# Kernel tuning notes

Hardware: AMD Instinct MI355X
Metric: run time of the kernel (lower is better)

## Reference

```python
import jax, jax.numpy as jnp
import numpy as np

B, L, D, H = 2, 2048, 1024, 16
DH = D // H
TAU = 0.1


def setup_inputs() -> dict:
    key = jax.random.key(0)
    ks = jax.random.split(key, 12)
    s = 0.02
    return {
        "q_x": jax.random.normal(ks[0], (B, L, D), jnp.float32),
        "k_x": jax.random.normal(ks[1], (B, L, D), jnp.float32),
        "v_x": jax.random.normal(ks[2], (B, L, D), jnp.float32),
        "ec": jax.random.normal(ks[3], (B, L, D), jnp.float32),
        "Wq": jax.random.normal(ks[4], (D, D), jnp.float32) * s,
        "bq": jnp.zeros((D,), jnp.float32),
        "Wk": jax.random.normal(ks[5], (D, D), jnp.float32) * s,
        "bk": jnp.zeros((D,), jnp.float32),
        "Wv": jax.random.normal(ks[6], (D, D), jnp.float32) * s,
        "bv": jnp.zeros((D,), jnp.float32),
        "Wo": jax.random.normal(ks[7], (D, D), jnp.float32) * s,
        "bo": jnp.zeros((D,), jnp.float32),
    }


def reference(q_x, k_x, v_x, ec, Wq, bq, Wk, bk, Wv, bv, Wo, bo):
    # torch nn.Linear: y = x @ W.T + b
    Q = (q_x @ Wq.T + bq).reshape(B, L, H, DH).transpose(0, 2, 1, 3)   # [B,H,L,Dh]
    K = (k_x @ Wk.T + bk).reshape(B, -1, H, DH).transpose(0, 2, 1, 3)  # [B,H,S,Dh]
    V = (v_x @ Wv.T + bv).reshape(B, -1, H, DH).transpose(0, 2, 1, 3)  # [B,H,S,Dh]
    scores = jnp.einsum("bhld,bhsd->bhls", Q, K) / jnp.sqrt(jnp.float32(DH))
    w = jnp.nan_to_num(jax.nn.softmax(scores, axis=-1), nan=0.0)       # [B,H,L,S]
    # frequency gate per key position: sigmoid((mean|ec| - tau) * 10)
    gate = jax.nn.sigmoid((jnp.abs(ec).mean(-1) - TAU) * 10.0)          # [B,S]
    w = w * gate[:, None, None, :]
    out = jnp.einsum("bhls,bhsd->bhld", w, V)                           # [B,H,L,Dh]
    out = out.transpose(0, 2, 1, 3).reshape(B, L, D)
    return out @ Wo.T + bo
```

## Files before the change

kernel.cpp:

```cpp
#include <hip/hip_runtime.h>

typedef unsigned short u16;
typedef unsigned int u32;
typedef unsigned long long u64;
typedef __attribute__((ext_vector_type(8))) short bf16x8;
typedef __attribute__((ext_vector_type(4))) float f32x4;
typedef __attribute__((ext_vector_type(2))) unsigned int u32x2;
typedef __attribute__((ext_vector_type(4))) unsigned int u32x4;

#define B_ 2
#define L_ 2048
#define D_ 1024
#define H_ 16
#define M_ 4096

__device__ __forceinline__ u16 f2bf(float f) {
  u32 x = __builtin_bit_cast(u32, f);
  return (u16)((x + 0x7fffu + ((x >> 16) & 1u)) >> 16);
}
__device__ __forceinline__ u32 cvtpk(float lo, float hi) {
  u32 r;
  asm("v_cvt_pk_bf16_f32 %0, %1, %2" : "=v"(r) : "v"(lo), "v"(hi));
  return r;
}

__device__ __forceinline__ void lane_regroup(u32& a, u32& b) {
#if __has_builtin(__builtin_amdgcn_permlane32_swap) && \
    __has_builtin(__builtin_amdgcn_permlane16_swap)
  u32x2 r = __builtin_amdgcn_permlane32_swap(a, b, false, false);
  u32x2 t = __builtin_amdgcn_permlane16_swap(r.x, r.y, false, false);
  a = t.x;
  b = t.y;
#else
  asm("v_permlane32_swap_b32 %0, %1\n\t"
      "v_permlane16_swap_b32 %0, %1"
      : "+v"(a), "+v"(b));
#endif
}

__device__ __forceinline__ void gl2lds16(void* lds, const void* g) {
  __builtin_amdgcn_global_load_lds(
      (const __attribute__((address_space(1))) u32*)g,
      (__attribute__((address_space(3))) u32*)lds, 16, 0, 0);
}

__device__ __forceinline__ void wait_vm8() {
  asm volatile("s_waitcnt vmcnt(8)" ::: "memory");
}
__device__ __forceinline__ void wait_vm0() {
  asm volatile("s_waitcnt vmcnt(0)" ::: "memory");
}
__device__ __forceinline__ void bar() {
  asm volatile("" ::: "memory");
  __builtin_amdgcn_s_barrier();
  asm volatile("" ::: "memory");
}

__global__ void cvt_all(const float* __restrict__ q, const float* __restrict__ k,
                        const float* __restrict__ v, const float* __restrict__ wq,
                        const float* __restrict__ wk, const float* __restrict__ wv,
                        const float* __restrict__ wo, const float* __restrict__ ec,
                        u16* __restrict__ Xq, u16* __restrict__ Xk, u16* __restrict__ Xv,
                        u16* __restrict__ Wqb, u16* __restrict__ Wkb,
                        u16* __restrict__ Wvb, u16* __restrict__ Wob,
                        float* __restrict__ gate) {
  if (blockIdx.x >= 16384) {
    int row = (blockIdx.x - 16384) * 4 + (threadIdx.x >> 6);
    int lane = threadIdx.x & 63;
    const float4* p = (const float4*)(ec + (size_t)row * 1024);
    float s = 0.f;
#pragma unroll
    for (int i = 0; i < 4; i++) {
      float4 vv = p[i * 64 + lane];
      s += fabsf(vv.x) + fabsf(vv.y) + fabsf(vv.z) + fabsf(vv.w);
    }
#pragma unroll
    for (int m = 1; m < 64; m <<= 1) s += __shfl_xor(s, m);
    if (lane == 0) {
      float mean = s * (1.0f / 1024.0f);
      gate[row] = 1.0f / (1.0f + __expf(-(mean - 0.1f) * 10.0f));
    }
    return;
  }
  int i = blockIdx.x * 256 + threadIdx.x;
  const float* s;
  u16* d;
  int off;
  if (i < 3145728) {
    int t = i >> 20;
    off = i & 1048575;
    s = t == 0 ? q : t == 1 ? k : v;
    d = t == 0 ? Xq : t == 1 ? Xk : Xv;
  } else {
    int j = i - 3145728;
    int t = j >> 18;
    off = j & 262143;
    s = t == 0 ? wq : t == 1 ? wk : t == 2 ? wv : wo;
    d = t == 0 ? Wqb : t == 1 ? Wkb : t == 2 ? Wvb : Wob;
  }
  float4 vv = ((const float4*)s)[off];
  ((u64*)d)[off] = (u64)cvtpk(vv.x, vv.y) | ((u64)cvtpk(vv.z, vv.w) << 32);
}

__global__ __launch_bounds__(256, 2) void gemm_qkv(
    const u16* __restrict__ Xq, const u16* __restrict__ Xk, const u16* __restrict__ Xv,
    const u16* __restrict__ Wq, const u16* __restrict__ Wk, const u16* __restrict__ Wv,
    const float* __restrict__ bq, const float* __restrict__ bk,
    const float* __restrict__ bv, const float* __restrict__ gate,
    u16* __restrict__ Qo, u16* __restrict__ Ko, u16* __restrict__ Vt) {
  __shared__ char smem[65536];
  const int which = blockIdx.x >> 8;
  const u16* A = which == 0 ? Xq : which == 1 ? Xk : Xv;
  const u16* Bw = which == 0 ? Wq : which == 1 ? Wk : Wv;
  const float* bias = which == 0 ? bq : which == 1 ? bk : bv;
  const int bi = blockIdx.x & 255;
  const int tid = threadIdx.x;
  const int tm = bi >> 3;
  const int tn = bi & 7;
  const int w = tid >> 6, lane = tid & 63;
  const int c = lane & 15, g = lane >> 4;
  const int wr = (w >> 1) << 6, wc = (w & 1) << 6;
  const int srow = tid >> 3, sch = tid & 7;

  f32x4 acc[4][4] = {};

  auto stage = [&](int buf, int t) {
    char* As = smem + buf * 32768;
    char* Bs = As + 16384;
#pragma unroll
    for (int i = 0; i < 4; i++) {
      int row = i * 32 + srow;
      int chs = (sch ^ (row & 7)) << 3;
      gl2lds16(As + i * 4096 + w * 1024, A + (size_t)(tm * 128 + row) * 1024 + t * 64 + chs);
      gl2lds16(Bs + i * 4096 + w * 1024, Bw + (size_t)(tn * 128 + row) * 1024 + t * 64 + chs);
    }
  };

  stage(0, 0);
  for (int t = 0; t < 16; t++) {
    int cur = t & 1;
    if (t < 15) {
      stage(cur ^ 1, t + 1);
      wait_vm8();
    } else {
      wait_vm0();
    }
    bar();
    const char* As = smem + cur * 32768;
    const char* Bs = As + 16384;
#pragma unroll
    for (int kd = 0; kd < 2; kd++) {
      bf16x8 af[4], bfr[4];
#pragma unroll
      for (int fi = 0; fi < 4; fi++) {
        int ra = wr + fi * 16 + c;
        af[fi] = *(const bf16x8*)(As + ra * 128 + ((((kd << 2) | g) ^ (ra & 7)) << 4));
        int rb = wc + fi * 16 + c;
        bfr[fi] = *(const bf16x8*)(Bs + rb * 128 + ((((kd << 2) | g) ^ (rb & 7)) << 4));
      }
#pragma unroll
      for (int fi = 0; fi < 4; fi++)
#pragma unroll
        for (int fj = 0; fj < 4; fj++)
          acc[fi][fj] = __builtin_amdgcn_mfma_f32_16x16x32_bf16(af[fi], bfr[fj],
                                                                acc[fi][fj], 0, 0, 0);
    }
    bar();
  }

  if (which == 2) {
    u16* T = (u16*)smem;
    __syncthreads();
#pragma unroll
    for (int fi = 0; fi < 4; fi++) {
      int lr0 = wr + fi * 16 + g * 4;
      float4 gg = *(const float4*)(gate + tm * 128 + lr0);
#pragma unroll
      for (int fj = 0; fj < 4; fj++) {
        int lc = wc + fj * 16 + c;
        float bv2 = bias[tn * 128 + lc];
        T[lc * 136 + lr0 + 0] = f2bf((acc[fi][fj][0] + bv2) * gg.x);
        T[lc * 136 + lr0 + 1] = f2bf((acc[fi][fj][1] + bv2) * gg.y);
        T[lc * 136 + lr0 + 2] = f2bf((acc[fi][fj][2] + bv2) * gg.z);
        T[lc * 136 + lr0 + 3] = f2bf((acc[fi][fj][3] + bv2) * gg.w);
      }
    }
    __syncthreads();
    const int lc = tid >> 1, hf = tid & 1;
    const int vtrow = (tm >> 4) * 1024 + tn * 128 + lc;
    const int s0 = (tm & 15) * 128 + hf * 64;
    const char* Trow = (const char*)(T + lc * 136) + hf * 128;
    u16* dst = Vt + (size_t)vtrow * 2048 + s0;
#pragma unroll
    for (int j = 0; j < 8; j++)
      *(bf16x8*)(dst + j * 8) = *(const bf16x8*)(Trow + j * 16);
  } else {
    u16* Cout = which == 0 ? Qo : Ko;
    const float oscl = which == 0 ? 0.18033688011112042f : 1.0f;
    const int rowb = tm * 128 + wr + g * 4;
    const int colb = tn * 128 + wc + c;
#pragma unroll
    for (int fj = 0; fj < 4; fj++) {
      int col = colb + fj * 16;
      float bv2 = bias[col];
#pragma unroll
      for (int fi = 0; fi < 4; fi++) {
        int r0 = rowb + fi * 16;
#pragma unroll
        for (int r = 0; r < 4; r++)
          Cout[(size_t)(r0 + r) * 1024 + col] = f2bf((acc[fi][fj][r] + bv2) * oscl);
      }
    }
  }
}

__global__ __launch_bounds__(256, 2) void gemm_o(const u16* __restrict__ A,
                                                 const u16* __restrict__ Bw,
                                                 const float* __restrict__ bias,
                                                 float* __restrict__ Cout) {
  __shared__ char smem[65536];
  const int tid = threadIdx.x;
  const int tm = blockIdx.x >> 3;
  const int tn = blockIdx.x & 7;
  const int w = tid >> 6, lane = tid & 63;
  const int c = lane & 15, g = lane >> 4;
  const int wr = (w >> 1) << 6, wc = (w & 1) << 6;
  const int srow = tid >> 3, sch = tid & 7;

  f32x4 acc[4][4] = {};

  auto stage = [&](int buf, int t) {
    char* As = smem + buf * 32768;
    char* Bs = As + 16384;
#pragma unroll
    for (int i = 0; i < 4; i++) {
      int row = i * 32 + srow;
      int chs = (sch ^ (row & 7)) << 3;
      gl2lds16(As + i * 4096 + w * 1024, A + (size_t)(tm * 128 + row) * 1024 + t * 64 + chs);
      gl2lds16(Bs + i * 4096 + w * 1024, Bw + (size_t)(tn * 128 + row) * 1024 + t * 64 + chs);
    }
  };

  stage(0, 0);
  for (int t = 0; t < 16; t++) {
    int cur = t & 1;
    if (t < 15) {
      stage(cur ^ 1, t + 1);
      wait_vm8();
    } else {
      wait_vm0();
    }
    bar();
    const char* As = smem + cur * 32768;
    const char* Bs = As + 16384;
#pragma unroll
    for (int kd = 0; kd < 2; kd++) {
      bf16x8 af[4], bfr[4];
#pragma unroll
      for (int fi = 0; fi < 4; fi++) {
        int ra = wr + fi * 16 + c;
        af[fi] = *(const bf16x8*)(As + ra * 128 + ((((kd << 2) | g) ^ (ra & 7)) << 4));
        int rb = wc + fi * 16 + c;
        bfr[fi] = *(const bf16x8*)(Bs + rb * 128 + ((((kd << 2) | g) ^ (rb & 7)) << 4));
      }
#pragma unroll
      for (int fi = 0; fi < 4; fi++)
#pragma unroll
        for (int fj = 0; fj < 4; fj++)
          acc[fi][fj] = __builtin_amdgcn_mfma_f32_16x16x32_bf16(af[fi], bfr[fj],
                                                                acc[fi][fj], 0, 0, 0);
    }
    bar();
  }

  const int rowb = tm * 128 + wr + g * 4;
  const int colb = tn * 128 + wc + c;
#pragma unroll
  for (int fj = 0; fj < 4; fj++) {
    int col = colb + fj * 16;
    float bv2 = bias[col];
#pragma unroll
    for (int fi = 0; fi < 4; fi++) {
      int r0 = rowb + fi * 16;
#pragma unroll
      for (int r = 0; r < 4; r++)
        Cout[(size_t)(r0 + r) * 1024 + col] = acc[fi][fj][r] + bv2;
    }
  }
}

__global__ __launch_bounds__(256, 2) void attn_kernel(const u16* __restrict__ Qb,
                                                      const u16* __restrict__ Kb,
                                                      const u16* __restrict__ Vt,
                                                      u16* __restrict__ Ob) {
  __shared__ char asmem[65536];
  const int bi = blockIdx.x;
  const int bh = (bi & 7) | ((bi >> 7) << 3);
  const int qt = (bi >> 3) & 15;
  const int b = bh >> 4, h = bh & 15;
  const int tid = threadIdx.x, w = tid >> 6, lane = tid & 63;
  const int c = lane & 15, g = lane >> 4;
  const int qrow0 = b * L_ + qt * 128 + w * 32;

  bf16x8 qf[2][2];
#pragma unroll
  for (int fj = 0; fj < 2; fj++)
#pragma unroll
    for (int kd = 0; kd < 2; kd++)
      qf[fj][kd] = *(const bf16x8*)(Qb + (size_t)(qrow0 + fj * 16 + c) * D_ + h * 64 +
                                    kd * 32 + g * 8);

  float lsum[2] = {0.f, 0.f};
  f32x4 oacc[4][2] = {};

  const int srow = tid >> 3, sch = tid & 7;
  const int vrow = tid >> 4, vch = tid & 15;

  auto stage = [&](int buf, int kv) {
    char* KsB = asmem + buf * 32768;
    char* VsB = KsB + 16384;
    int sbase = kv * 128;
#pragma unroll
    for (int i = 0; i < 4; i++) {
      int kr = i * 32 + srow;
      gl2lds16(KsB + i * 4096 + w * 1024,
               Kb + (size_t)(b * L_ + sbase + kr) * D_ + h * 64 + ((sch ^ (kr & 7)) << 3));
      int vr = i * 16 + vrow;
      gl2lds16(VsB + i * 4096 + w * 1024,
               Vt + (size_t)(bh * 64 + vr) * 2048 + sbase + ((vch ^ (vr & 15)) << 3));
    }
  };

  stage(0, 0);
  for (int kv = 0; kv < 16; kv++) {
    int cur = kv & 1;
    if (kv < 15) {
      stage(cur ^ 1, kv + 1);
      wait_vm8();
    } else {
      wait_vm0();
    }
    bar();
    const char* Ks = asmem + cur * 32768;
    const char* Vs = Ks + 16384;

    f32x4 st0[8] = {}, st1[8] = {};
    __builtin_amdgcn_s_setprio(1);
#pragma unroll
    for (int kd = 0; kd < 2; kd++) {
#pragma unroll
      for (int fi = 0; fi < 8; fi++) {
        int row = fi * 16 + c;
        bf16x8 kf = *(const bf16x8*)(Ks + row * 128 + ((((kd << 2) | g) ^ (c & 7)) << 4));
        st0[fi] = __builtin_amdgcn_mfma_f32_16x16x32_bf16(kf, qf[0][kd], st0[fi], 0, 0, 0);
        st1[fi] = __builtin_amdgcn_mfma_f32_16x16x32_bf16(kf, qf[1][kd], st1[fi], 0, 0, 0);
      }
    }
    __builtin_amdgcn_s_setprio(0);

    u32 pkA0[8], pkB0[8], pkA1[8], pkB1[8];
    float rs0 = 0.f, rs1 = 0.f;
#pragma unroll
    for (int fi = 0; fi < 8; fi++) {
      float p0 = __builtin_amdgcn_exp2f(st0[fi][0]);
      float p1 = __builtin_amdgcn_exp2f(st0[fi][1]);
      float p2 = __builtin_amdgcn_exp2f(st0[fi][2]);
      float p3 = __builtin_amdgcn_exp2f(st0[fi][3]);
      rs0 += (p0 + p1) + (p2 + p3);
      pkA0[fi] = cvtpk(p0, p1);
      pkB0[fi] = cvtpk(p2, p3);
    }
#pragma unroll
    for (int fi = 0; fi < 8; fi++) {
      float p0 = __builtin_amdgcn_exp2f(st1[fi][0]);
      float p1 = __builtin_amdgcn_exp2f(st1[fi][1]);
      float p2 = __builtin_amdgcn_exp2f(st1[fi][2]);
      float p3 = __builtin_amdgcn_exp2f(st1[fi][3]);
      rs1 += (p0 + p1) + (p2 + p3);
      pkA1[fi] = cvtpk(p0, p1);
      pkB1[fi] = cvtpk(p2, p3);
    }
    lsum[0] += rs0;
    lsum[1] += rs1;

    __builtin_amdgcn_s_setprio(1);
#pragma unroll
    for (int ks = 0; ks < 4; ks++) {
      u32 a0 = pkA0[2 * ks], b0 = pkA0[2 * ks + 1];
      lane_regroup(a0, b0);
      u32 a1 = pkB0[2 * ks], b1 = pkB0[2 * ks + 1];
      lane_regroup(a1, b1);
      u32x4 pw0 = {a0, a1, b0, b1};
      bf16x8 pf0 = __builtin_bit_cast(bf16x8, pw0);
      u32 e0 = pkA1[2 * ks], f0 = pkA1[2 * ks + 1];
      lane_regroup(e0, f0);
      u32 e1 = pkB1[2 * ks], f1 = pkB1[2 * ks + 1];
      lane_regroup(e1, f1);
      u32x4 pw1 = {e0, e1, f0, f1};
      bf16x8 pf1 = __builtin_bit_cast(bf16x8, pw1);
#pragma unroll
      for (int fd = 0; fd < 4; fd++) {
        int vr2 = fd * 16 + c;
        bf16x8 vf = *(const bf16x8*)(Vs + vr2 * 256 + ((((ks << 2) | g) ^ (vr2 & 15)) << 4));
        oacc[fd][0] = __builtin_amdgcn_mfma_f32_16x16x32_bf16(vf, pf0, oacc[fd][0], 0, 0, 0);
        oacc[fd][1] = __builtin_amdgcn_mfma_f32_16x16x32_bf16(vf, pf1, oacc[fd][1], 0, 0, 0);
      }
    }
    __builtin_amdgcn_s_setprio(0);
    bar();
  }

#pragma unroll
  for (int fj = 0; fj < 2; fj++) {
    lsum[fj] += __shfl_xor(lsum[fj], 16);
    lsum[fj] += __shfl_xor(lsum[fj], 32);
    float inv = 1.0f / lsum[fj];
    size_t orow = (size_t)(qrow0 + fj * 16 + c) * D_ + h * 64;
#pragma unroll
    for (int fd = 0; fd < 4; fd++) {
      u64 pk = (u64)cvtpk(oacc[fd][fj][0] * inv, oacc[fd][fj][1] * inv) |
               ((u64)cvtpk(oacc[fd][fj][2] * inv, oacc[fd][fj][3] * inv) << 32);
      *(u64*)(Ob + orow + fd * 16 + g * 4) = pk;
    }
  }
}

extern "C" void kernel_launch(void* const* d_in, const int* in_sizes, int n_in,
                              void* d_out, int out_size, void* d_ws, size_t ws_size,
                              hipStream_t stream) {
  const float* q_x = (const float*)d_in[0];
  const float* k_x = (const float*)d_in[1];
  const float* v_x = (const float*)d_in[2];
  const float* ec = (const float*)d_in[3];
  const float* Wq = (const float*)d_in[4];
  const float* bq = (const float*)d_in[5];
  const float* Wk = (const float*)d_in[6];
  const float* bk = (const float*)d_in[7];
  const float* Wv = (const float*)d_in[8];
  const float* bv = (const float*)d_in[9];
  const float* Wo = (const float*)d_in[10];
  const float* bo = (const float*)d_in[11];

  char* ws = (char*)d_ws;
  const size_t MB = 1024 * 1024;
  u16* Wqb = (u16*)(ws + 0 * MB);
  u16* Wkb = (u16*)(ws + 2 * MB);
  u16* Wvb = (u16*)(ws + 4 * MB);
  u16* Wob = (u16*)(ws + 6 * MB);
  float* gatep = (float*)(ws + 8 * MB);
  u16* Xq = (u16*)(ws + 9 * MB);
  u16* Xk = (u16*)(ws + 17 * MB);
  u16* Xv = (u16*)(ws + 25 * MB);
  u16* Qb = (u16*)(ws + 33 * MB);
  u16* Kb = (u16*)(ws + 41 * MB);
  u16* Vtb = (u16*)(ws + 49 * MB);
  u16* Ab = Xk;

  cvt_all<<<17408, 256, 0, stream>>>(q_x, k_x, v_x, Wq, Wk, Wv, Wo, ec, Xq, Xk, Xv,
                                     Wqb, Wkb, Wvb, Wob, gatep);
  gemm_qkv<<<768, 256, 0, stream>>>(Xq, Xk, Xv, Wqb, Wkb, Wvb, bq, bk, bv, gatep, Qb,
                                    Kb, Vtb);
  attn_kernel<<<512, 256, 0, stream>>>(Qb, Kb, Vtb, Ab);
  gemm_o<<<256, 256, 0, stream>>>(Ab, Wob, bo, (float*)d_out);
}
```

Measured before the change: 115.5 us.

## Halve gemm_o M-tile and compute softmax row sums with ones-MFMA

The output projection GEMM now uses 64x128 tiles with 512 blocks instead of 128x128 tiles with 256 blocks, so more CUs are busy on the 4096x1024 output. Its LDS use and per-wave accumulators shrink, and the vmcnt wait threshold is adjusted to match. In attention, the per-lane exp row-sum accumulation and the cross-lane shuffles are replaced by an extra MFMA per step that multiplies the bf16 probabilities by a vector of ones. This takes VALU adds off the softmax path but sums the bf16-rounded probabilities, which changes numerics slightly, and it reduces reuse of the GEMM tile.

```diff
diff --git a/kernel.cpp b/kernel.cpp
--- a/kernel.cpp
+++ b/kernel.cpp
@@ -46,6 +46,9 @@
 
 __device__ __forceinline__ void wait_vm8() {
   asm volatile("s_waitcnt vmcnt(8)" ::: "memory");
+}
+__device__ __forceinline__ void wait_vm6() {
+  asm volatile("s_waitcnt vmcnt(6)" ::: "memory");
 }
 __device__ __forceinline__ void wait_vm0() {
   asm volatile("s_waitcnt vmcnt(0)" ::: "memory");
@@ -218,25 +221,31 @@
                                                  const u16* __restrict__ Bw,
                                                  const float* __restrict__ bias,
                                                  float* __restrict__ Cout) {
-  __shared__ char smem[65536];
+  __shared__ char smem[49152];
   const int tid = threadIdx.x;
   const int tm = blockIdx.x >> 3;
   const int tn = blockIdx.x & 7;
   const int w = tid >> 6, lane = tid & 63;
   const int c = lane & 15, g = lane >> 4;
-  const int wr = (w >> 1) << 6, wc = (w & 1) << 6;
+  const int wr = (w >> 1) << 5;
+  const int wc = (w & 1) << 6;
   const int srow = tid >> 3, sch = tid & 7;
 
-  f32x4 acc[4][4] = {};
+  f32x4 acc[2][4] = {};
 
   auto stage = [&](int buf, int t) {
-    char* As = smem + buf * 32768;
-    char* Bs = As + 16384;
+    char* As = smem + buf * 24576;
+    char* Bs = As + 8192;
+#pragma unroll
+    for (int i = 0; i < 2; i++) {
+      int row = i * 32 + srow;
+      int chs = (sch ^ (row & 7)) << 3;
+      gl2lds16(As + i * 4096 + w * 1024, A + (size_t)(tm * 64 + row) * 1024 + t * 64 + chs);
+    }
 #pragma unroll
     for (int i = 0; i < 4; i++) {
       int row = i * 32 + srow;
       int chs = (sch ^ (row & 7)) << 3;
-      gl2lds16(As + i * 4096 + w * 1024, A + (size_t)(tm * 128 + row) * 1024 + t * 64 + chs);
       gl2lds16(Bs + i * 4096 + w * 1024, Bw + (size_t)(tn * 128 + row) * 1024 + t * 64 + chs);
     }
   };
@@ -246,25 +255,28 @@
     int cur = t & 1;
     if (t < 15) {
       stage(cur ^ 1, t + 1);
-      wait_vm8();
+      wait_vm6();
     } else {
       wait_vm0();
     }
     bar();
-    const char* As = smem + cur * 32768;
-    const char* Bs = As + 16384;
+    const char* As = smem + cur * 24576;
+    const char* Bs = As + 8192;
 #pragma unroll
     for (int kd = 0; kd < 2; kd++) {
-      bf16x8 af[4], bfr[4];
-#pragma unroll
-      for (int fi = 0; fi < 4; fi++) {
+      bf16x8 af[2], bfr[4];
+#pragma unroll
+      for (int fi = 0; fi < 2; fi++) {
         int ra = wr + fi * 16 + c;
         af[fi] = *(const bf16x8*)(As + ra * 128 + ((((kd << 2) | g) ^ (ra & 7)) << 4));
-        int rb = wc + fi * 16 + c;
-        bfr[fi] = *(const bf16x8*)(Bs + rb * 128 + ((((kd << 2) | g) ^ (rb & 7)) << 4));
-      }
-#pragma unroll
-      for (int fi = 0; fi < 4; fi++)
+      }
+#pragma unroll
+      for (int fj = 0; fj < 4; fj++) {
+        int rb = wc + fj * 16 + c;
+        bfr[fj] = *(const bf16x8*)(Bs + rb * 128 + ((((kd << 2) | g) ^ (rb & 7)) << 4));
+      }
+#pragma unroll
+      for (int fi = 0; fi < 2; fi++)
 #pragma unroll
         for (int fj = 0; fj < 4; fj++)
           acc[fi][fj] = __builtin_amdgcn_mfma_f32_16x16x32_bf16(af[fi], bfr[fj],
@@ -273,14 +285,14 @@
     bar();
   }
 
-  const int rowb = tm * 128 + wr + g * 4;
+  const int rowb = tm * 64 + wr + g * 4;
   const int colb = tn * 128 + wc + c;
 #pragma unroll
   for (int fj = 0; fj < 4; fj++) {
     int col = colb + fj * 16;
     float bv2 = bias[col];
 #pragma unroll
-    for (int fi = 0; fi < 4; fi++) {
+    for (int fi = 0; fi < 2; fi++) {
       int r0 = rowb + fi * 16;
 #pragma unroll
       for (int r = 0; r < 4; r++)
@@ -310,8 +322,11 @@
       qf[fj][kd] = *(const bf16x8*)(Qb + (size_t)(qrow0 + fj * 16 + c) * D_ + h * 64 +
                                     kd * 32 + g * 8);
 
-  float lsum[2] = {0.f, 0.f};
+  const u32x4 onew = {0x3F803F80u, 0x3F803F80u, 0x3F803F80u, 0x3F803F80u};
+  const bf16x8 one8 = __builtin_bit_cast(bf16x8, onew);
+
   f32x4 oacc[4][2] = {};
+  f32x4 oaccD[2] = {};
 
   const int srow = tid >> 3, sch = tid & 7;
   const int vrow = tid >> 4, vch = tid & 15;
@@ -359,29 +374,16 @@
     __builtin_amdgcn_s_setprio(0);
 
     u32 pkA0[8], pkB0[8], pkA1[8], pkB1[8];
-    float rs0 = 0.f, rs1 = 0.f;
 #pragma unroll
     for (int fi = 0; fi < 8; fi++) {
-      float p0 = __builtin_amdgcn_exp2f(st0[fi][0]);
-      float p1 = __builtin_amdgcn_exp2f(st0[fi][1]);
-      float p2 = __builtin_amdgcn_exp2f(st0[fi][2]);
-      float p3 = __builtin_amdgcn_exp2f(st0[fi][3]);
-      rs0 += (p0 + p1) + (p2 + p3);
-      pkA0[fi] = cvtpk(p0, p1);
-      pkB0[fi] = cvtpk(p2, p3);
+      pkA0[fi] = cvtpk(__builtin_amdgcn_exp2f(st0[fi][0]), __builtin_amdgcn_exp2f(st0[fi][1]));
+      pkB0[fi] = cvtpk(__builtin_amdgcn_exp2f(st0[fi][2]), __builtin_amdgcn_exp2f(st0[fi][3]));
     }
 #pragma unroll
     for (int fi = 0; fi < 8; fi++) {
-      float p0 = __builtin_amdgcn_exp2f(st1[fi][0]);
-      float p1 = __builtin_amdgcn_exp2f(st1[fi][1]);
-      float p2 = __builtin_amdgcn_exp2f(st1[fi][2]);
-      float p3 = __builtin_amdgcn_exp2f(st1[fi][3]);
-      rs1 += (p0 + p1) + (p2 + p3);
-      pkA1[fi] = cvtpk(p0, p1);
-      pkB1[fi] = cvtpk(p2, p3);
-    }
-    lsum[0] += rs0;
-    lsum[1] += rs1;
+      pkA1[fi] = cvtpk(__builtin_amdgcn_exp2f(st1[fi][0]), __builtin_amdgcn_exp2f(st1[fi][1]));
+      pkB1[fi] = cvtpk(__builtin_amdgcn_exp2f(st1[fi][2]), __builtin_amdgcn_exp2f(st1[fi][3]));
+    }
 
     __builtin_amdgcn_s_setprio(1);
 #pragma unroll
@@ -398,6 +400,8 @@
       lane_regroup(e1, f1);
       u32x4 pw1 = {e0, e1, f0, f1};
       bf16x8 pf1 = __builtin_bit_cast(bf16x8, pw1);
+      oaccD[0] = __builtin_amdgcn_mfma_f32_16x16x32_bf16(one8, pf0, oaccD[0], 0, 0, 0);
+      oaccD[1] = __builtin_amdgcn_mfma_f32_16x16x32_bf16(one8, pf1, oaccD[1], 0, 0, 0);
 #pragma unroll
       for (int fd = 0; fd < 4; fd++) {
         int vr2 = fd * 16 + c;
@@ -412,9 +416,7 @@
 
 #pragma unroll
   for (int fj = 0; fj < 2; fj++) {
-    lsum[fj] += __shfl_xor(lsum[fj], 16);
-    lsum[fj] += __shfl_xor(lsum[fj], 32);
-    float inv = 1.0f / lsum[fj];
+    float inv = 1.0f / oaccD[fj][0];
     size_t orow = (size_t)(qrow0 + fj * 16 + c) * D_ + h * 64;
 #pragma unroll
     for (int fd = 0; fd < 4; fd++) {
@@ -461,5 +463,5 @@
   gemm_qkv<<<768, 256, 0, stream>>>(Xq, Xk, Xv, Wqb, Wkb, Wvb, bq, bk, bv, gatep, Qb,
                                     Kb, Vtb);
   attn_kernel<<<512, 256, 0, stream>>>(Qb, Kb, Vtb, Ab);
-  gemm_o<<<256, 256, 0, stream>>>(Ab, Wob, bo, (float*)d_out);
-}
+  gemm_o<<<512, 256, 0, stream>>>(Ab, Wob, bo, (float*)d_out);
+}
```

Result: no change. 114.3 us (-1.1%).
